# Optimization experiments

Hardware: AMD Instinct MI355X
Metric: run time of the kernel (lower is better)

## Reference

```python
import jax, jax.numpy as jnp
import numpy as np

N_EMBD = 1024
N_HEAD = 16
HEAD_DIM = N_EMBD // N_HEAD

def setup_inputs() -> dict:
    key = jax.random.key(0)
    ks = jax.random.split(key, 9)
    B, T, C = 2, 2048, N_EMBD
    s = 1.0 / np.sqrt(C)
    x = jax.random.normal(ks[0], (B, T, C), dtype=jnp.float32)
    Wk = jax.random.normal(ks[1], (C, C), dtype=jnp.float32) * s
    bk = jnp.zeros((C,), dtype=jnp.float32)
    Wq = jax.random.normal(ks[2], (C, C), dtype=jnp.float32) * s
    bq = jnp.zeros((C,), dtype=jnp.float32)
    Wv = jax.random.normal(ks[3], (C, C), dtype=jnp.float32) * s
    bv = jnp.zeros((C,), dtype=jnp.float32)
    Wp = jax.random.normal(ks[4], (C, C), dtype=jnp.float32) * s
    bp = jnp.zeros((C,), dtype=jnp.float32)
    return {"x": x, "Wq": Wq, "bq": bq, "Wk": Wk, "bk": bk, "Wv": Wv, "bv": bv, "Wp": Wp, "bp": bp}

def reference(x, Wq, bq, Wk, bk, Wv, bv, Wp, bp):
    B, T, C = x.shape
    H, D = N_HEAD, HEAD_DIM
    # QKV projections (torch Linear: x @ W.T + b; here W is stored as (in,out))
    q = (x @ Wq + bq).reshape(B, T, H, D).transpose(0, 2, 1, 3)  # [B,H,T,D]
    k = (x @ Wk + bk).reshape(B, T, H, D).transpose(0, 2, 1, 3)
    v = (x @ Wv + bv).reshape(B, T, H, D).transpose(0, 2, 1, 3)
    att = jnp.einsum('bhtd,bhsd->bhts', q, k) / jnp.sqrt(jnp.float32(D))
    causal = jnp.tril(jnp.ones((T, T), dtype=bool))
    att = jnp.where(causal, att, jnp.float32(-jnp.inf))
    att = jax.nn.softmax(att, axis=-1)
    y = jnp.einsum('bhts,bhsd->bhtd', att, v)  # [B,H,T,D]
    y = y.transpose(0, 2, 1, 3).reshape(B, T, C)
    return y @ Wp + bp
```

## Files before the change

kernel.cpp:

```cpp
#include <hip/hip_runtime.h>
#include <cstdint>

typedef __attribute__((ext_vector_type(4))) short s16x4;
typedef __attribute__((ext_vector_type(8))) short s16x8;
typedef __attribute__((ext_vector_type(4))) float f32x4;
typedef __attribute__((ext_vector_type(16))) float f32x16;

#define L2E 1.44269504088896340736f

__device__ __forceinline__ short f2bf(float f) {
  union { float f; unsigned u; } v; v.f = f;
  unsigned r = (v.u + 0x7fffu + ((v.u >> 16) & 1u)) >> 16;
  return (short)r;
}

__device__ __forceinline__ float xhalf_f(float x) {
  union { float f; unsigned u; } a; a.f = x;
  auto r = __builtin_amdgcn_permlane32_swap(a.u, a.u, false, false);
  union { unsigned u; float f; } b;
  b.u = (threadIdx.x & 32) ? r[0] : r[1];
  return b.f;
}

typedef const __attribute__((address_space(1))) unsigned int* gas_p;
typedef __attribute__((address_space(3))) unsigned int* las_p;
__device__ __forceinline__ void stage16(const void* g, void* l) {
  __builtin_amdgcn_global_load_lds((gas_p)(uintptr_t)g,
                                   (las_p)(unsigned int)(uintptr_t)l, 16, 0, 0);
}

__global__ __launch_bounds__(256) void prepass(const float* __restrict__ W0,
                                               const float* __restrict__ W1,
                                               const float* __restrict__ W2,
                                               const float* __restrict__ W3,
                                               short* __restrict__ wdst,
                                               const float* __restrict__ x,
                                               short* __restrict__ xb) {
  const int z = blockIdx.z;
  const int t = threadIdx.x;
  if (z >= 4) {
    int i = ((z - 4) * 256 + blockIdx.y * 16 + blockIdx.x) * 256 + t;
    const f32x4* p = (const f32x4*)x + (size_t)i * 2;
    f32x4 a = p[0], b = p[1];
    s16x8 o;
    o[0] = f2bf(a[0]); o[1] = f2bf(a[1]); o[2] = f2bf(a[2]); o[3] = f2bf(a[3]);
    o[4] = f2bf(b[0]); o[5] = f2bf(b[1]); o[6] = f2bf(b[2]); o[7] = f2bf(b[3]);
    *((s16x8*)xb + i) = o;
    return;
  }
  __shared__ float tile[64][65];
  const float* in = (z == 0) ? W0 : (z == 1) ? W1 : (z == 2) ? W2 : W3;
  short* out = wdst + (size_t)z * 1048576;
  const int bi = blockIdx.y, bj = blockIdx.x;
  const int c = t & 63, r0 = t >> 6;
#pragma unroll
  for (int i = 0; i < 16; i++) {
    int r = r0 + i * 4;
    tile[r][c] = in[(size_t)(bi * 64 + r) * 1024 + bj * 64 + c];
  }
  __syncthreads();
#pragma unroll
  for (int i = 0; i < 16; i++) {
    int r = r0 + i * 4;
    out[(size_t)(bj * 64 + r) * 1024 + bi * 64 + c] = f2bf(tile[c][r]);
  }
}

template <int EPI, int BM>
__global__ __launch_bounds__(BM * 2) void gemm_bt(
    const short* __restrict__ A, const short* __restrict__ B, int N, int K,
    const float* __restrict__ b0, const float* __restrict__ b1,
    const float* __restrict__ b2, short* __restrict__ o0, short* __restrict__ o1,
    short* __restrict__ o2, float* __restrict__ ofp) {
  constexpr int T = BM * 2;
  constexpr int AR = 2;
  constexpr int BR = 512 / T;
  constexpr int BUFB = (BM + 128) * 32;
  __shared__ short L[2 * BUFB];
  const int tid = threadIdx.x;
  const int lane = tid & 63;
  const int wave = tid >> 6;
  const int wr = wave >> 1, wc = wave & 1;
  const int l15 = lane & 15, l4 = lane >> 4;
  const int id = blockIdx.x + gridDim.x * blockIdx.y;
  const int cpx = gridDim.x >> 3;
  const int xcd = id & 7, sub = id >> 3;
  const int m0 = (sub / cpx) * BM;
  const int n0 = (xcd * cpx + sub % cpx) * 128;
  f32x4 acc[4][4];
#pragma unroll
  for (int i = 0; i < 4; i++)
#pragma unroll
    for (int j = 0; j < 4; j++) acc[i][j] = (f32x4){0.f, 0.f, 0.f, 0.f};

  const int lq = tid & 3, lr = tid >> 2;
  int soffA[AR], goffA[AR];
#pragma unroll
  for (int i = 0; i < AR; i++) {
    const int r = i * (T / 4) + lr;
    soffA[i] = r * 32 + lq * 8;
    goffA[i] = r * K + lq * 8;
  }
  int soffB[BR], goffB[BR];
#pragma unroll
  for (int j = 0; j < BR; j++) {
    const int r = j * (T / 4) + lr;
    soffB[j] = BM * 32 + r * 32 + lq * 8;
    goffB[j] = r * K + lq * 8;
  }

  const short* Asrc = A + (size_t)m0 * K;
  const short* Bsrc = B + (size_t)n0 * K;
  short* bufC = L;
  short* bufN = L + BUFB;

#define GSTAGE(BUF)                                                            \
  {                                                                            \
    _Pragma("unroll") for (int i_ = 0; i_ < AR; i_++)                          \
        stage16(Asrc + goffA[i_], (BUF) + soffA[i_]);                          \
    _Pragma("unroll") for (int j_ = 0; j_ < BR; j_++)                          \
        stage16(Bsrc + goffB[j_], (BUF) + soffB[j_]);                          \
    Asrc += 32; Bsrc += 32;                                                    \
  }

  GSTAGE(bufC)
  const int NK = K >> 5;
  for (int kt = 0; kt < NK; kt++) {
    __syncthreads();
    if (kt + 1 < NK) GSTAGE(bufN)
    s16x8 af[4], bfr[4];
#pragma unroll
    for (int i = 0; i < 4; i++) {
      af[i] = *(const s16x8*)(bufC + (wr * 64 + i * 16 + l15) * 32 + l4 * 8);
      bfr[i] = *(const s16x8*)(bufC + BM * 32 + (wc * 64 + i * 16 + l15) * 32 + l4 * 8);
    }
#pragma unroll
    for (int mi = 0; mi < 4; mi++)
#pragma unroll
      for (int ni = 0; ni < 4; ni++)
        acc[mi][ni] = __builtin_amdgcn_mfma_f32_16x16x32_bf16(af[mi], bfr[ni],
                                                              acc[mi][ni], 0, 0, 0);
    short* t_ = bufC; bufC = bufN; bufN = t_;
  }
#undef GSTAGE

#pragma unroll
  for (int ni = 0; ni < 4; ni++) {
    const int col = n0 + wc * 64 + ni * 16 + l15;
    if (EPI == 1) {
      const float bias = b0[col];
#pragma unroll
      for (int mi = 0; mi < 4; mi++)
#pragma unroll
        for (int r = 0; r < 4; r++) {
          int row = m0 + wr * 64 + mi * 16 + l4 * 4 + r;
          ofp[(size_t)row * N + col] = acc[mi][ni][r] + bias;
        }
    } else {
      const float* bp; short* dst; int c1; int isV = 0; float scl = 1.0f;
      if (col < 1024) { bp = b0; dst = o0; c1 = col; scl = 0.125f * L2E; }
      else if (col < 2048) { bp = b1; dst = o1; c1 = col - 1024; }
      else { bp = b2; dst = o2; c1 = col - 2048; isV = 1; }
      const float bias = bp[c1];
      const int h = c1 >> 6, d = c1 & 63;
      if (isV) {
#pragma unroll
        for (int mi = 0; mi < 4; mi++) {
          int t0 = m0 + wr * 64 + mi * 16 + l4 * 4;
          int bb = t0 >> 11, t = t0 & 2047;
          s16x4 ov;
#pragma unroll
          for (int r = 0; r < 4; r++) ov[r] = f2bf(acc[mi][ni][r] + bias);
          *(s16x4*)(dst + (size_t)((bb * 16 + h) * 64 + d) * 2048 + t) = ov;
        }
      } else {
#pragma unroll
        for (int mi = 0; mi < 4; mi++)
#pragma unroll
          for (int r = 0; r < 4; r++) {
            int row = m0 + wr * 64 + mi * 16 + l4 * 4 + r;
            int bb = row >> 11, t = row & 2047;
            float v = (acc[mi][ni][r] + bias) * scl;
            dst[(size_t)((bb * 16 + h) * 2048 + t) * 64 + d] = f2bf(v);
          }
      }
    }
  }
}

__global__ __launch_bounds__(128) void attn_v8(const short* __restrict__ Q,
                                               const short* __restrict__ K,
                                               const short* __restrict__ Vt,
                                               short* __restrict__ Y) {
  __shared__ short Ks[2][64 * 64];
  __shared__ short Vs[3][64 * 64];
  const int bh = blockIdx.x;
  const int y = blockIdx.y;
  const int g = y >> 3, r_ = y & 7;
  const int qbase = (g << 3) | ((g & 1) ? (7 - r_) : r_);
  const int qt = (qbase + ((bh & 3) << 3)) & 31;
  const int tid = threadIdx.x, lane = tid & 63, wave = tid >> 6;
  const int q31 = lane & 31, hi = lane >> 5;
  const short* Qp = Q + (size_t)bh * 2048 * 64;
  const short* Kp = K + (size_t)bh * 2048 * 64;
  const short* Vp = Vt + (size_t)bh * 64 * 2048;
  const int qrow = qt * 64 + wave * 32 + q31;
  const int nt = qt + 1;
  const int cx = q31 & 7;

  s16x8 qf[4];
#pragma unroll
  for (int s = 0; s < 4; s++)
    qf[s] = *(const s16x8*)(Qp + (size_t)qrow * 64 + s * 16 + hi * 8);

  f32x16 accA, accB, Z;
#pragma unroll
  for (int i = 0; i < 16; i++) { accA[i] = 0.f; accB[i] = 0.f; Z[i] = 0.f; }
  float l = 0.f;

  const int srow = tid >> 3, sch = tid & 7;
  int sdst[4], koff[4], voff[4];
#pragma unroll
  for (int i = 0; i < 4; i++) {
    const int r = srow + i * 16;
    const int sc = sch ^ (r & 7);
    sdst[i] = r * 64 + sch * 8;
    koff[i] = r * 64 + sc * 8;
    voff[i] = r * 2048 + sc * 8;
  }
  const short* kst = Kp;
  const short* vst = Vp;
  int rd0[4];
#pragma unroll
  for (int s = 0; s < 4; s++) rd0[s] = q31 * 64 + (((2 * s + hi) ^ cx) << 3);

  short* kA = &Ks[0][0]; short* kB = &Ks[1][0];
  short* vP = &Vs[2][0]; short* vC = &Vs[0][0]; short* vN = &Vs[1][0];

#pragma unroll
  for (int i = 0; i < 4; i++) {
    stage16(kst + koff[i], kA + sdst[i]);
    stage16(vst + voff[i], vC + sdst[i]);
  }
  kst += 4096; vst += 64;

#define STAGE_NEXT(COND)                                                       \
  if (COND) {                                                                  \
    _Pragma("unroll") for (int i_ = 0; i_ < 4; i_++) {                         \
      stage16(kst + koff[i_], kB + sdst[i_]);                                  \
      stage16(vst + voff[i_], vN + sdst[i_]);                                  \
    }                                                                          \
    kst += 4096; vst += 64;                                                    \
  }

#define QK(S0, S1)                                                             \
  {                                                                            \
    s16x8 kf0_[4], kf1_[4];                                                    \
    _Pragma("unroll") for (int s_ = 0; s_ < 4; s_++) {                         \
      kf0_[s_] = *(const s16x8*)(kA + rd0[s_]);                                \
      kf1_[s_] = *(const s16x8*)(kA + rd0[s_] + 2048);                         \
    }                                                                          \
    __builtin_amdgcn_s_setprio(1);                                             \
    S0 = __builtin_amdgcn_mfma_f32_32x32x16_bf16(kf0_[0], qf[0], Z, 0, 0, 0);  \
    S1 = __builtin_amdgcn_mfma_f32_32x32x16_bf16(kf1_[0], qf[0], Z, 0, 0, 0);  \
    _Pragma("unroll") for (int s_ = 1; s_ < 4; s_++) {                         \
      S0 = __builtin_amdgcn_mfma_f32_32x32x16_bf16(kf0_[s_], qf[s_], S0, 0, 0, 0); \
      S1 = __builtin_amdgcn_mfma_f32_32x32x16_bf16(kf1_[s_], qf[s_], S1, 0, 0, 0); \
    }                                                                          \
    __builtin_amdgcn_s_setprio(0);                                             \
  }

#define SMPV_BODY(S0, S1)                                                      \
  {                                                                            \
    float rsum_ = 0.f;                                                         \
    _Pragma("unroll") for (int r2_ = 0; r2_ < 16; r2_++) {                     \
      float p_ = __builtin_amdgcn_exp2f(S0[r2_]);                              \
      S0[r2_] = p_; rsum_ += p_;                                               \
    }                                                                          \
    _Pragma("unroll") for (int r2_ = 0; r2_ < 16; r2_++) {                     \
      float p_ = __builtin_amdgcn_exp2f(S1[r2_]);                              \
      S1[r2_] = p_; rsum_ += p_;                                               \
    }                                                                          \
    l += rsum_;                                                                \
    unsigned pk0_[8], pk1_[8];                                                 \
    _Pragma("unroll") for (int j_ = 0; j_ < 8; j_++) {                         \
      unsigned u_;                                                             \
      float a0_ = S0[2 * j_], a1_ = S0[2 * j_ + 1];                            \
      asm("v_cvt_pk_bf16_f32 %0, %1, %2" : "=v"(u_) : "v"(a0_), "v"(a1_));     \
      pk0_[j_] = u_;                                                           \
      float b0_ = S1[2 * j_], b1_ = S1[2 * j_ + 1];                            \
      asm("v_cvt_pk_bf16_f32 %0, %1, %2" : "=v"(u_) : "v"(b0_), "v"(b1_));     \
      pk1_[j_] = u_;                                                           \
    }                                                                          \
    _Pragma("unroll") for (int s_ = 0; s_ < 4; s_++) {                         \
      const unsigned* pk_ = (s_ < 2) ? pk0_ : pk1_;                            \
      const int b_ = 4 * (s_ & 1);                                             \
      auto rA_ = __builtin_amdgcn_permlane32_swap(pk_[b_ + 0], pk_[b_ + 2], false, false); \
      auto rB_ = __builtin_amdgcn_permlane32_swap(pk_[b_ + 1], pk_[b_ + 3], false, false); \
      union { unsigned u[4]; s16x8 v; } fr_;                                   \
      fr_.u[0] = rA_[0]; fr_.u[1] = rB_[0]; fr_.u[2] = rA_[1]; fr_.u[3] = rB_[1]; \
      s16x8 vf0_ = *(const s16x8*)(vP + rd0[s_]);                              \
      s16x8 vf1_ = *(const s16x8*)(vP + rd0[s_] + 2048);                       \
      __builtin_amdgcn_s_setprio(1);                                           \
      accA = __builtin_amdgcn_mfma_f32_32x32x16_bf16(vf0_, fr_.v, accA, 0, 0, 0); \
      accB = __builtin_amdgcn_mfma_f32_32x32x16_bf16(vf1_, fr_.v, accB, 0, 0, 0); \
      __builtin_amdgcn_s_setprio(0);                                           \
    }                                                                          \
  }

#define SMPV_MASK(S0, S1)                                                      \
  {                                                                            \
    const int k0_ = (nt - 1) * 64;                                             \
    _Pragma("unroll") for (int r2_ = 0; r2_ < 16; r2_++) {                     \
      int kvr_ = k0_ + (r2_ & 3) + 8 * (r2_ >> 2) + 4 * hi;                    \
      if (kvr_ > qrow) S0[r2_] = -__builtin_inff();                            \
      if (kvr_ + 32 > qrow) S1[r2_] = -__builtin_inff();                       \
    }                                                                          \
    SMPV_BODY(S0, S1)                                                          \
  }

#define ROT()                                                                  \
  {                                                                            \
    short* t_ = kA; kA = kB; kB = t_;                                          \
    t_ = vP; vP = vC; vC = vN; vN = t_;                                        \
  }

  f32x16 sA0, sA1, sB0, sB1;
  __syncthreads();
  STAGE_NEXT(nt > 1)
  QK(sA0, sA1)
  ROT()
  int t = 1;
  for (; t + 1 < nt; t += 2) {
    __syncthreads();
    STAGE_NEXT(t + 1 < nt)
    QK(sB0, sB1)
    SMPV_BODY(sA0, sA1)
    ROT()
    __syncthreads();
    STAGE_NEXT(t + 2 < nt)
    QK(sA0, sA1)
    SMPV_BODY(sB0, sB1)
    ROT()
  }
  if (t < nt) {
    __syncthreads();
    QK(sB0, sB1)
    SMPV_BODY(sA0, sA1)
    ROT()
    SMPV_MASK(sB0, sB1)
  } else {
    SMPV_MASK(sA0, sA1)
  }
#undef STAGE_NEXT
#undef QK
#undef SMPV_BODY
#undef SMPV_MASK
#undef ROT

  const int b_ = bh >> 4, h_ = bh & 15;
  const float lt = l + xhalf_f(l);
  const float invl = 1.f / lt;
  const size_t base = ((size_t)b_ * 2048 + qrow) * 1024 + h_ * 64;
#pragma unroll
  for (int gg = 0; gg < 4; gg++) {
    s16x4 o0, o1;
#pragma unroll
    for (int e = 0; e < 4; e++) {
      o0[e] = f2bf(accA[4 * gg + e] * invl);
      o1[e] = f2bf(accB[4 * gg + e] * invl);
    }
    *(s16x4*)(Y + base + 8 * gg + 4 * hi) = o0;
    *(s16x4*)(Y + base + 32 + 8 * gg + 4 * hi) = o1;
  }
}

extern "C" void kernel_launch(void* const* d_in, const int* in_sizes, int n_in,
                              void* d_out, int out_size, void* d_ws, size_t ws_size,
                              hipStream_t stream) {
  const float* x = (const float*)d_in[0];
  const float* Wq = (const float*)d_in[1];
  const float* bq = (const float*)d_in[2];
  const float* Wk = (const float*)d_in[3];
  const float* bk = (const float*)d_in[4];
  const float* Wv = (const float*)d_in[5];
  const float* bv = (const float*)d_in[6];
  const float* Wp = (const float*)d_in[7];
  const float* bp = (const float*)d_in[8];
  float* out = (float*)d_out;
  char* ws = (char*)d_ws;

  short* xb    = (short*)(ws + 0);
  short* WqkvT = (short*)(ws + 8388608);
  short* WpT   = (short*)(ws + 14680064);
  short* Qb    = (short*)(ws + 16777216);
  short* Kb    = (short*)(ws + 25165824);
  short* Vtb   = (short*)(ws + 33554432);
  short* Yb    = xb;

  prepass<<<dim3(16, 16, 12), 256, 0, stream>>>(Wq, Wk, Wv, Wp, WqkvT, x, xb);
  gemm_bt<0, 128><<<dim3(24, 32), 256, 0, stream>>>(xb, WqkvT, 3072, 1024, bq, bk,
                                                    bv, Qb, Kb, Vtb, nullptr);
  attn_v8<<<dim3(32, 32), 128, 0, stream>>>(Qb, Kb, Vtb, Yb);
  gemm_bt<1, 64><<<dim3(8, 64), 128, 0, stream>>>(Yb, WpT, 1024, 1024, bp, nullptr,
                                                  nullptr, nullptr, nullptr,
                                                  nullptr, out);
}
```

Baseline: 106.1 us.

## Fuse x fp32-to-bf16 conversion into QKV GEMM and split softmax row-sum

Drops the separate pass that converted x to bf16. A dedicated QKV GEMM now stages fp32 x tiles into LDS with an XOR swizzle and converts them to bf16 in registers before the MFMAs. This saves writing and re-reading the bf16 copy of x, but the A tile doubles in LDS and global traffic per k-step, and each step adds conversion instructions. Separately, the attention softmax row-sum now uses four partial accumulators to break its serial dependency chain.

```diff
diff --git a/kernel.cpp b/kernel.cpp
--- a/kernel.cpp
+++ b/kernel.cpp
@@ -33,21 +33,9 @@
                                                const float* __restrict__ W1,
                                                const float* __restrict__ W2,
                                                const float* __restrict__ W3,
-                                               short* __restrict__ wdst,
-                                               const float* __restrict__ x,
-                                               short* __restrict__ xb) {
+                                               short* __restrict__ wdst) {
   const int z = blockIdx.z;
   const int t = threadIdx.x;
-  if (z >= 4) {
-    int i = ((z - 4) * 256 + blockIdx.y * 16 + blockIdx.x) * 256 + t;
-    const f32x4* p = (const f32x4*)x + (size_t)i * 2;
-    f32x4 a = p[0], b = p[1];
-    s16x8 o;
-    o[0] = f2bf(a[0]); o[1] = f2bf(a[1]); o[2] = f2bf(a[2]); o[3] = f2bf(a[3]);
-    o[4] = f2bf(b[0]); o[5] = f2bf(b[1]); o[6] = f2bf(b[2]); o[7] = f2bf(b[3]);
-    *((s16x8*)xb + i) = o;
-    return;
-  }
   __shared__ float tile[64][65];
   const float* in = (z == 0) ? W0 : (z == 1) ? W1 : (z == 2) ? W2 : W3;
   short* out = wdst + (size_t)z * 1048576;
@@ -66,12 +54,135 @@
   }
 }
 
-template <int EPI, int BM>
+__global__ __launch_bounds__(256) void gemm_qkv(
+    const float* __restrict__ A, const short* __restrict__ B,
+    const float* __restrict__ b0, const float* __restrict__ b1,
+    const float* __restrict__ b2, short* __restrict__ o0,
+    short* __restrict__ o1, short* __restrict__ o2) {
+  constexpr int K = 1024;
+  constexpr int BUFB = 24576;
+  __shared__ char L[2 * BUFB];
+  const int tid = threadIdx.x;
+  const int lane = tid & 63;
+  const int wave = tid >> 6;
+  const int wr = wave >> 1, wc = wave & 1;
+  const int l15 = lane & 15, l4 = lane >> 4;
+  const int id = blockIdx.x + gridDim.x * blockIdx.y;
+  const int cpx = gridDim.x >> 3;
+  const int xcd = id & 7, sub = id >> 3;
+  const int m0 = (sub / cpx) * 128;
+  const int n0 = (xcd * cpx + sub % cpx) * 128;
+  f32x4 acc[4][4];
+#pragma unroll
+  for (int i = 0; i < 4; i++)
+#pragma unroll
+    for (int j = 0; j < 4; j++) acc[i][j] = (f32x4){0.f, 0.f, 0.f, 0.f};
+
+  int sA[4], gA[4];
+#pragma unroll
+  for (int i = 0; i < 4; i++) {
+    const int r = i * 32 + (tid >> 3);
+    const int ch = tid & 7;
+    sA[i] = (i * 256 + tid) * 16;
+    gA[i] = r * K + ((ch ^ (r & 7)) << 2);
+  }
+  int sB[2], gB[2];
+#pragma unroll
+  for (int j = 0; j < 2; j++) {
+    const int flat = j * 256 + tid;
+    sB[j] = 16384 + flat * 16;
+    gB[j] = (flat >> 2) * K + (flat & 3) * 8;
+  }
+  int abase[4];
+#pragma unroll
+  for (int i = 0; i < 4; i++) {
+    const int row = wr * 64 + i * 16 + l15;
+    const int c0 = ((l4 << 1) ^ (l15 & 7));
+    abase[i] = row * 128 + (c0 << 4);
+  }
+  const int bbase = 16384 + (wc * 64 + l15) * 64 + l4 * 16;
+
+  const float* Asrc = A + (size_t)m0 * K;
+  const short* Bsrc = B + (size_t)n0 * K;
+  char* bufC = L;
+  char* bufN = L + BUFB;
+
+#define GSTAGE(BUF)                                                            \
+  {                                                                            \
+    _Pragma("unroll") for (int i_ = 0; i_ < 4; i_++)                           \
+        stage16(Asrc + gA[i_], (BUF) + sA[i_]);                                \
+    _Pragma("unroll") for (int j_ = 0; j_ < 2; j_++)                           \
+        stage16(Bsrc + gB[j_], (BUF) + sB[j_]);                                \
+    Asrc += 32; Bsrc += 32;                                                    \
+  }
+
+  GSTAGE(bufC)
+  const int NK = K >> 5;
+  for (int kt = 0; kt < NK; kt++) {
+    __syncthreads();
+    if (kt + 1 < NK) GSTAGE(bufN)
+    s16x8 af[4], bfr[4];
+#pragma unroll
+    for (int i = 0; i < 4; i++) {
+      f32x4 a0 = *(const f32x4*)(bufC + abase[i]);
+      f32x4 a1 = *(const f32x4*)(bufC + (abase[i] ^ 16));
+      unsigned u0, u1, u2, u3;
+      asm("v_cvt_pk_bf16_f32 %0, %1, %2" : "=v"(u0) : "v"(a0[0]), "v"(a0[1]));
+      asm("v_cvt_pk_bf16_f32 %0, %1, %2" : "=v"(u1) : "v"(a0[2]), "v"(a0[3]));
+      asm("v_cvt_pk_bf16_f32 %0, %1, %2" : "=v"(u2) : "v"(a1[0]), "v"(a1[1]));
+      asm("v_cvt_pk_bf16_f32 %0, %1, %2" : "=v"(u3) : "v"(a1[2]), "v"(a1[3]));
+      union { unsigned u[4]; s16x8 v; } fr;
+      fr.u[0] = u0; fr.u[1] = u1; fr.u[2] = u2; fr.u[3] = u3;
+      af[i] = fr.v;
+      bfr[i] = *(const s16x8*)(bufC + bbase + i * 1024);
+    }
+#pragma unroll
+    for (int mi = 0; mi < 4; mi++)
+#pragma unroll
+      for (int ni = 0; ni < 4; ni++)
+        acc[mi][ni] = __builtin_amdgcn_mfma_f32_16x16x32_bf16(af[mi], bfr[ni],
+                                                              acc[mi][ni], 0, 0, 0);
+    char* t_ = bufC; bufC = bufN; bufN = t_;
+  }
+#undef GSTAGE
+
+#pragma unroll
+  for (int ni = 0; ni < 4; ni++) {
+    const int col = n0 + wc * 64 + ni * 16 + l15;
+    const float* bp; short* dst; int c1; int isV = 0; float scl = 1.0f;
+    if (col < 1024) { bp = b0; dst = o0; c1 = col; scl = 0.125f * L2E; }
+    else if (col < 2048) { bp = b1; dst = o1; c1 = col - 1024; }
+    else { bp = b2; dst = o2; c1 = col - 2048; isV = 1; }
+    const float bias = bp[c1];
+    const int h = c1 >> 6, d = c1 & 63;
+    if (isV) {
+#pragma unroll
+      for (int mi = 0; mi < 4; mi++) {
+        int t0 = m0 + wr * 64 + mi * 16 + l4 * 4;
+        int bb = t0 >> 11, t = t0 & 2047;
+        s16x4 ov;
+#pragma unroll
+        for (int r = 0; r < 4; r++) ov[r] = f2bf(acc[mi][ni][r] + bias);
+        *(s16x4*)(dst + (size_t)((bb * 16 + h) * 64 + d) * 2048 + t) = ov;
+      }
+    } else {
+#pragma unroll
+      for (int mi = 0; mi < 4; mi++)
+#pragma unroll
+        for (int r = 0; r < 4; r++) {
+          int row = m0 + wr * 64 + mi * 16 + l4 * 4 + r;
+          int bb = row >> 11, t = row & 2047;
+          float v = (acc[mi][ni][r] + bias) * scl;
+          dst[(size_t)((bb * 16 + h) * 2048 + t) * 64 + d] = f2bf(v);
+        }
+    }
+  }
+}
+
+template <int BM>
 __global__ __launch_bounds__(BM * 2) void gemm_bt(
     const short* __restrict__ A, const short* __restrict__ B, int N, int K,
-    const float* __restrict__ b0, const float* __restrict__ b1,
-    const float* __restrict__ b2, short* __restrict__ o0, short* __restrict__ o1,
-    short* __restrict__ o2, float* __restrict__ ofp) {
+    const float* __restrict__ b0, float* __restrict__ ofp) {
   constexpr int T = BM * 2;
   constexpr int AR = 2;
   constexpr int BR = 512 / T;
@@ -147,44 +258,14 @@
 #pragma unroll
   for (int ni = 0; ni < 4; ni++) {
     const int col = n0 + wc * 64 + ni * 16 + l15;
-    if (EPI == 1) {
-      const float bias = b0[col];
-#pragma unroll
-      for (int mi = 0; mi < 4; mi++)
-#pragma unroll
-        for (int r = 0; r < 4; r++) {
-          int row = m0 + wr * 64 + mi * 16 + l4 * 4 + r;
-          ofp[(size_t)row * N + col] = acc[mi][ni][r] + bias;
-        }
-    } else {
-      const float* bp; short* dst; int c1; int isV = 0; float scl = 1.0f;
-      if (col < 1024) { bp = b0; dst = o0; c1 = col; scl = 0.125f * L2E; }
-      else if (col < 2048) { bp = b1; dst = o1; c1 = col - 1024; }
-      else { bp = b2; dst = o2; c1 = col - 2048; isV = 1; }
-      const float bias = bp[c1];
-      const int h = c1 >> 6, d = c1 & 63;
-      if (isV) {
-#pragma unroll
-        for (int mi = 0; mi < 4; mi++) {
-          int t0 = m0 + wr * 64 + mi * 16 + l4 * 4;
-          int bb = t0 >> 11, t = t0 & 2047;
-          s16x4 ov;
-#pragma unroll
-          for (int r = 0; r < 4; r++) ov[r] = f2bf(acc[mi][ni][r] + bias);
-          *(s16x4*)(dst + (size_t)((bb * 16 + h) * 64 + d) * 2048 + t) = ov;
-        }
-      } else {
-#pragma unroll
-        for (int mi = 0; mi < 4; mi++)
-#pragma unroll
-          for (int r = 0; r < 4; r++) {
-            int row = m0 + wr * 64 + mi * 16 + l4 * 4 + r;
-            int bb = row >> 11, t = row & 2047;
-            float v = (acc[mi][ni][r] + bias) * scl;
-            dst[(size_t)((bb * 16 + h) * 2048 + t) * 64 + d] = f2bf(v);
-          }
+    const float bias = b0[col];
+#pragma unroll
+    for (int mi = 0; mi < 4; mi++)
+#pragma unroll
+      for (int r = 0; r < 4; r++) {
+        int row = m0 + wr * 64 + mi * 16 + l4 * 4 + r;
+        ofp[(size_t)row * N + col] = acc[mi][ni][r] + bias;
       }
-    }
   }
 }
 
@@ -272,16 +353,20 @@
 
 #define SMPV_BODY(S0, S1)                                                      \
   {                                                                            \
-    float rsum_ = 0.f;                                                         \
+    float rs0_ = 0.f, rs1_ = 0.f, rs2_ = 0.f, rs3_ = 0.f;                      \
     _Pragma("unroll") for (int r2_ = 0; r2_ < 16; r2_++) {                     \
       float p_ = __builtin_amdgcn_exp2f(S0[r2_]);                              \
-      S0[r2_] = p_; rsum_ += p_;                                               \
+      S0[r2_] = p_;                                                            \
+      if ((r2_ & 3) == 0) rs0_ += p_; else if ((r2_ & 3) == 1) rs1_ += p_;     \
+      else if ((r2_ & 3) == 2) rs2_ += p_; else rs3_ += p_;                    \
     }                                                                          \
     _Pragma("unroll") for (int r2_ = 0; r2_ < 16; r2_++) {                     \
       float p_ = __builtin_amdgcn_exp2f(S1[r2_]);                              \
-      S1[r2_] = p_; rsum_ += p_;                                               \
-    }                                                                          \
-    l += rsum_;                                                                \
+      S1[r2_] = p_;                                                            \
+      if ((r2_ & 3) == 0) rs0_ += p_; else if ((r2_ & 3) == 1) rs1_ += p_;     \
+      else if ((r2_ & 3) == 2) rs2_ += p_; else rs3_ += p_;                    \
+    }                                                                          \
+    l += (rs0_ + rs1_) + (rs2_ + rs3_);                                        \
     unsigned pk0_[8], pk1_[8];                                                 \
     _Pragma("unroll") for (int j_ = 0; j_ < 8; j_++) {                         \
       unsigned u_;                                                             \
@@ -390,19 +475,15 @@
   float* out = (float*)d_out;
   char* ws = (char*)d_ws;
 
-  short* xb    = (short*)(ws + 0);
+  short* Yb    = (short*)(ws + 0);
   short* WqkvT = (short*)(ws + 8388608);
   short* WpT   = (short*)(ws + 14680064);
   short* Qb    = (short*)(ws + 16777216);
   short* Kb    = (short*)(ws + 25165824);
   short* Vtb   = (short*)(ws + 33554432);
-  short* Yb    = xb;
-
-  prepass<<<dim3(16, 16, 12), 256, 0, stream>>>(Wq, Wk, Wv, Wp, WqkvT, x, xb);
-  gemm_bt<0, 128><<<dim3(24, 32), 256, 0, stream>>>(xb, WqkvT, 3072, 1024, bq, bk,
-                                                    bv, Qb, Kb, Vtb, nullptr);
+
+  prepass<<<dim3(16, 16, 4), 256, 0, stream>>>(Wq, Wk, Wv, Wp, WqkvT);
+  gemm_qkv<<<dim3(24, 32), 256, 0, stream>>>(x, WqkvT, bq, bk, bv, Qb, Kb, Vtb);
   attn_v8<<<dim3(32, 32), 128, 0, stream>>>(Qb, Kb, Vtb, Yb);
-  gemm_bt<1, 64><<<dim3(8, 64), 128, 0, stream>>>(Yb, WpT, 1024, 1024, bp, nullptr,
-                                                  nullptr, nullptr, nullptr,
-                                                  nullptr, out);
-}
+  gemm_bt<64><<<dim3(8, 64), 128, 0, stream>>>(Yb, WpT, 1024, 1024, bp, out);
+}
```

Result: slower. 113.3 us (+6.8%).
